# Kernel tuning notes

Measured on AMD Instinct MI355X. Metric: run time of the kernel, lower is better.

The kernel has to match this reference:

```python
import jax, jax.numpy as jnp
import numpy as np

B, N, E = 128, 50000, 1600000


def setup_inputs() -> dict:
    key = jax.random.key(0)
    k1, k2, k3, k4, k5 = jax.random.split(key, 5)
    x = jax.random.normal(k1, (B, N), dtype=jnp.float32)
    h = jax.random.normal(k2, (N,), dtype=jnp.float32)
    J = jax.random.normal(k3, (E,), dtype=jnp.float32)
    edge_idx_i = jax.random.randint(k4, (E,), 0, N, dtype=jnp.int64) if jax.config.jax_enable_x64 else jax.random.randint(k4, (E,), 0, N, dtype=jnp.int32)
    edge_idx_j = jax.random.randint(k5, (E,), 0, N, dtype=jnp.int32)
    return {"x": x, "h": h, "J": J, "edge_idx_i": edge_idx_i, "edge_idx_j": edge_idx_j}


def reference(x, h, J, edge_idx_i, edge_idx_j):
    # Hamiltonian: H(x) = x @ h + (x[:, ei] * x[:, ej]) @ J  -> shape (B,)
    interactions = x[:, edge_idx_i] * x[:, edge_idx_j]  # (B, E)
    return x @ h + interactions @ J
```

## Files before the change

### kernel.cpp

```cpp
#include <hip/hip_runtime.h>
#include <hip/hip_bf16.h>
#include <hip/hip_fp16.h>

#define BDIM    128
#define NGROUPS 2
#define GCOLS   64
#define ROWB    (GCOLS * 2)
#define EBLK    2048
#define RANKS   (EBLK / NGROUPS)
#define CHUNK   256
#define S1BLK   (NGROUPS * 8)
#define HBLK2   8
#define RPS     (RANKS / 8)
#define TPAD    132

__global__ __launch_bounds__(256) void transpose_h_kernel(
    const float* __restrict__ x, const float* __restrict__ h,
    __half* __restrict__ xTh, float* __restrict__ hp, int N) {
  __shared__ float tile[64 * TPAD];
  __shared__ float sh[64];
  __shared__ float red2[2][BDIM];
  const int tid = threadIdx.x;
  const int n0  = blockIdx.x * 64;

  const int c     = tid & 15;
  const int b0    = tid >> 4;
  const int nbase = n0 + 4 * c;
#pragma unroll
  for (int p = 0; p < 8; ++p) {
    const int b = b0 + 16 * p;
    float4 v;
    if (nbase + 3 < N) {
      v = *(const float4*)&x[(size_t)b * N + nbase];
    } else {
      v.x = (nbase + 0 < N) ? x[(size_t)b * N + nbase + 0] : 0.f;
      v.y = (nbase + 1 < N) ? x[(size_t)b * N + nbase + 1] : 0.f;
      v.z = (nbase + 2 < N) ? x[(size_t)b * N + nbase + 2] : 0.f;
      v.w = (nbase + 3 < N) ? x[(size_t)b * N + nbase + 3] : 0.f;
    }
    tile[(4 * c + 0) * TPAD + b] = v.x;
    tile[(4 * c + 1) * TPAD + b] = v.y;
    tile[(4 * c + 2) * TPAD + b] = v.z;
    tile[(4 * c + 3) * TPAD + b] = v.w;
  }
  if (tid < 64) sh[tid] = (n0 + tid < N) ? h[n0 + tid] : 0.f;
  __syncthreads();

  const int hb   = tid & 127;
  const int half = tid >> 7;
  float hacc = 0.f;
#pragma unroll
  for (int m = 0; m < 32; ++m) {
    const int nl = half * 32 + m;
    hacc += tile[nl * TPAD + hb] * sh[nl];
  }
  red2[half][hb] = hacc;

  const int oct = tid & 7;
  const int g2  = (tid >> 3) & 1;
  const int r0  = tid >> 4;
#pragma unroll
  for (int p = 0; p < 4; ++p) {
    const int nl = r0 + 16 * p;
    const int n  = n0 + nl;
    if (n < N) {
      const float* src = &tile[nl * TPAD + g2 * GCOLS + oct * 8];
      const float4 lo = *(const float4*)(src);
      const float4 hi = *(const float4*)(src + 4);
      int4 outv;
      outv.x = __builtin_bit_cast(int, __floats2half2_rn(lo.x, lo.y));
      outv.y = __builtin_bit_cast(int, __floats2half2_rn(lo.z, lo.w));
      outv.z = __builtin_bit_cast(int, __floats2half2_rn(hi.x, hi.y));
      outv.w = __builtin_bit_cast(int, __floats2half2_rn(hi.z, hi.w));
      *(int4*)(xTh + ((size_t)g2 * N + n) * GCOLS + oct * 8) = outv;
    }
  }
  __syncthreads();
  if (tid < BDIM) hp[(size_t)blockIdx.x * BDIM + tid] = red2[0][tid] + red2[1][tid];
}

__device__ __forceinline__ void fma8mix(float* acc, int4 vi, int4 vj, float Jv) {
  const int wi[4] = {vi.x, vi.y, vi.z, vi.w};
  const int wj[4] = {vj.x, vj.y, vj.z, vj.w};
#pragma unroll
  for (int w = 0; w < 4; ++w) {
    const __half2 hi = __builtin_bit_cast(__half2, wi[w]);
    const __half2 hj = __builtin_bit_cast(__half2, wj[w]);
    const int p = __builtin_bit_cast(int, __hmul2(hi, hj));
    asm("v_fma_mix_f32 %0, %1, %2, %0 op_sel_hi:[1,0,0]"
        : "+v"(acc[2 * w]) : "v"(p), "v"(Jv));
    asm("v_fma_mix_f32 %0, %1, %2, %0 op_sel:[1,0,0] op_sel_hi:[1,0,0]"
        : "+v"(acc[2 * w + 1]) : "v"(p), "v"(Jv));
  }
}

__global__ __launch_bounds__(256, 4) void edge_kernel(
    const __half* __restrict__ xTh, const float* __restrict__ J,
    const int* __restrict__ ei, const int* __restrict__ ej,
    float* __restrict__ P, int E, int N) {
  const int tid  = threadIdx.x;
  const int g    = (blockIdx.x & 7) >> 2;
  const int rank = (blockIdx.x >> 3) * 4 + (blockIdx.x & 3);
  const int wave = tid >> 6;
  const int lane = tid & 63;
  const int k    = lane >> 3;
  const char* xgl = (const char*)xTh + (size_t)g * N * ROWB + (lane & 7) * 16;

  const int TC    = (E + CHUNK - 1) / CHUNK;
  const int start = (int)(((long)rank * TC / RANKS)) * CHUNK;
  const int end   = min((int)(((long)(rank + 1) * TC / RANKS)) * CHUNK, E);

  __shared__ int4 se[CHUNK];

  int ri = 0, rj = 0;
  float rJ = 0.f;
  {
    const int e = start + tid;
    if (e < end) { ri = ei[e]; rj = ej[e]; rJ = J[e]; }
  }

  float acc[8] = {0.f, 0.f, 0.f, 0.f, 0.f, 0.f, 0.f, 0.f};

  for (int base = start; base < end; base += CHUNK) {
    se[tid] = make_int4(ri, rj, __float_as_int(rJ), 0);
    __syncthreads();

    {
      const int e = base + CHUNK + tid;
      ri = 0; rj = 0; rJ = 0.f;
      if (e < end) { ri = ei[e]; rj = ej[e]; rJ = J[e]; }
    }

    const int lbase = wave * 64 + k;
    const int4 eA0 = se[lbase + 0 * 8];
    const int4 eA1 = se[lbase + 1 * 8];
    const int4 eA2 = se[lbase + 2 * 8];
    const int4 eA3 = se[lbase + 3 * 8];
    const int4 viA0 = *(const int4*)(xgl + (unsigned)eA0.x * ROWB);
    const int4 vjA0 = *(const int4*)(xgl + (unsigned)eA0.y * ROWB);
    const int4 viA1 = *(const int4*)(xgl + (unsigned)eA1.x * ROWB);
    const int4 vjA1 = *(const int4*)(xgl + (unsigned)eA1.y * ROWB);
    const int4 viA2 = *(const int4*)(xgl + (unsigned)eA2.x * ROWB);
    const int4 vjA2 = *(const int4*)(xgl + (unsigned)eA2.y * ROWB);
    const int4 viA3 = *(const int4*)(xgl + (unsigned)eA3.x * ROWB);
    const int4 vjA3 = *(const int4*)(xgl + (unsigned)eA3.y * ROWB);
    const int4 eB0 = se[lbase + 4 * 8];
    const int4 eB1 = se[lbase + 5 * 8];
    const int4 eB2 = se[lbase + 6 * 8];
    const int4 eB3 = se[lbase + 7 * 8];
    const int4 viB0 = *(const int4*)(xgl + (unsigned)eB0.x * ROWB);
    const int4 vjB0 = *(const int4*)(xgl + (unsigned)eB0.y * ROWB);
    const int4 viB1 = *(const int4*)(xgl + (unsigned)eB1.x * ROWB);
    const int4 vjB1 = *(const int4*)(xgl + (unsigned)eB1.y * ROWB);
    const int4 viB2 = *(const int4*)(xgl + (unsigned)eB2.x * ROWB);
    const int4 vjB2 = *(const int4*)(xgl + (unsigned)eB2.y * ROWB);
    const int4 viB3 = *(const int4*)(xgl + (unsigned)eB3.x * ROWB);
    const int4 vjB3 = *(const int4*)(xgl + (unsigned)eB3.y * ROWB);
    __builtin_amdgcn_sched_barrier(0);
    fma8mix(acc, viA0, vjA0, __int_as_float(eA0.z));
    fma8mix(acc, viA1, vjA1, __int_as_float(eA1.z));
    fma8mix(acc, viA2, vjA2, __int_as_float(eA2.z));
    fma8mix(acc, viA3, vjA3, __int_as_float(eA3.z));
    fma8mix(acc, viB0, vjB0, __int_as_float(eB0.z));
    fma8mix(acc, viB1, vjB1, __int_as_float(eB1.z));
    fma8mix(acc, viB2, vjB2, __int_as_float(eB2.z));
    fma8mix(acc, viB3, vjB3, __int_as_float(eB3.z));
    __syncthreads();
  }

#pragma unroll
  for (int off = 8; off < 64; off <<= 1)
#pragma unroll
    for (int w = 0; w < 8; ++w) acc[w] += __shfl_xor(acc[w], off);

  __shared__ float red[4][GCOLS];
  if (lane < 8)
#pragma unroll
    for (int w = 0; w < 8; ++w) red[wave][lane * 8 + w] = acc[w];
  __syncthreads();
  if (tid < GCOLS) {
    const float s = red[0][tid] + red[1][tid] + red[2][tid] + red[3][tid];
    P[((size_t)g * RANKS + rank) * GCOLS + tid] = s;
  }
}

__global__ __launch_bounds__(256) void reduce1_kernel(
    const float* __restrict__ P, const float* __restrict__ hp,
    float* __restrict__ P2, float* __restrict__ hp2, int hrows) {
  __shared__ float red[4][GCOLS];
  __shared__ float redh[2][BDIM];
  if (blockIdx.x < S1BLK) {
    const int g  = blockIdx.x >> 3;
    const int s  = blockIdx.x & 7;
    const int rl = threadIdx.x >> 6;
    const int c  = threadIdx.x & 63;
    float acc = 0.f;
    for (int rr = rl; rr < RPS; rr += 4)
      acc += P[((size_t)g * RANKS + s * RPS + rr) * GCOLS + c];
    red[rl][c] = acc;
    __syncthreads();
    if (threadIdx.x < GCOLS) {
      float sum = 0.f;
      for (int r = 0; r < 4; ++r) sum += red[r][threadIdx.x];
      P2[(size_t)blockIdx.x * GCOLS + threadIdx.x] = sum;
    }
  } else {
    const int s  = blockIdx.x - S1BLK;
    const int b  = threadIdx.x & 127;
    const int rg = threadIdx.x >> 7;
    float acc = 0.f;
    for (int r = s + 8 * rg; r < hrows; r += 16)
      acc += hp[(size_t)r * BDIM + b];
    redh[rg][b] = acc;
    __syncthreads();
    if (threadIdx.x < BDIM)
      hp2[(size_t)s * BDIM + threadIdx.x] = redh[0][threadIdx.x] + redh[1][threadIdx.x];
  }
}

__global__ __launch_bounds__(128) void reduce2_kernel(
    const float* __restrict__ P2, const float* __restrict__ hp2,
    float* __restrict__ out) {
  const int b = threadIdx.x;
  const int g = b >> 6;
  const int c = b & 63;
  float acc = 0.f;
  for (int s = 0; s < 8; ++s) acc += hp2[(size_t)s * BDIM + b];
  for (int s = 0; s < 8; ++s) acc += P2[(size_t)(g * 8 + s) * GCOLS + c];
  out[b] = acc;
}

extern "C" void kernel_launch(void* const* d_in, const int* in_sizes, int n_in,
                              void* d_out, int out_size, void* d_ws, size_t ws_size,
                              hipStream_t stream) {
  const float* x  = (const float*)d_in[0];
  const float* h  = (const float*)d_in[1];
  const float* J  = (const float*)d_in[2];
  const int*   ei = (const int*)d_in[3];
  const int*   ej = (const int*)d_in[4];
  float* out = (float*)d_out;

  const int N = in_sizes[1];
  const int E = in_sizes[2];

  const int tblocks = (N + 63) / 64;

  __half* xTh = (__half*)d_ws;
  float* P   = (float*)(xTh + (size_t)NGROUPS * N * GCOLS);
  float* P2  = P   + (size_t)NGROUPS * RANKS * GCOLS;
  float* hp  = P2  + (size_t)S1BLK * GCOLS;
  float* hp2 = hp  + (size_t)tblocks * BDIM;

  transpose_h_kernel<<<tblocks, 256, 0, stream>>>(x, h, xTh, hp, N);

  edge_kernel<<<EBLK, 256, 0, stream>>>(xTh, J, ei, ej, P, E, N);

  reduce1_kernel<<<S1BLK + HBLK2, 256, 0, stream>>>(P, hp, P2, hp2, tblocks);

  reduce2_kernel<<<1, BDIM, 0, stream>>>(P2, hp2, out);
}
```

Baseline: 80.81 us.

## Partition edges per wave and broadcast indices via shuffles instead of LDS

Each wave now owns its own contiguous range of 64-edge chunks instead of the block sharing 256-edge chunks staged through shared memory. Edge indices and weights are prefetched into registers per lane and distributed with wave shuffles, which removes the LDS staging and both __syncthreads per iteration. This lets waves progress independently and avoids barrier stalls. The cost is 24 shuffles per iteration and finer-grained load balance that may leave some waves with one more chunk than others.

```diff
diff --git a/kernel.cpp b/kernel.cpp
--- a/kernel.cpp
+++ b/kernel.cpp
@@ -8,7 +8,7 @@
 #define ROWB    (GCOLS * 2)
 #define EBLK    2048
 #define RANKS   (EBLK / NGROUPS)
-#define CHUNK   256
+#define WPG     (RANKS * 4)
 #define S1BLK   (NGROUPS * 8)
 #define HBLK2   8
 #define RPS     (RANKS / 8)
@@ -106,66 +106,71 @@
   const int k    = lane >> 3;
   const char* xgl = (const char*)xTh + (size_t)g * N * ROWB + (lane & 7) * 16;
 
-  const int TC    = (E + CHUNK - 1) / CHUNK;
-  const int start = (int)(((long)rank * TC / RANKS)) * CHUNK;
-  const int end   = min((int)(((long)(rank + 1) * TC / RANKS)) * CHUNK, E);
-
-  __shared__ int4 se[CHUNK];
+  const int  wi   = rank * 4 + wave;
+  const long TC   = (E + 63) >> 6;
+  int base = (int)((long)wi * TC / WPG) * 64;
+  const int bend = (int)((long)(wi + 1) * TC / WPG) * 64;
+
+  float acc[8] = {0.f, 0.f, 0.f, 0.f, 0.f, 0.f, 0.f, 0.f};
 
   int ri = 0, rj = 0;
   float rJ = 0.f;
-  {
-    const int e = start + tid;
-    if (e < end) { ri = ei[e]; rj = ej[e]; rJ = J[e]; }
-  }
-
-  float acc[8] = {0.f, 0.f, 0.f, 0.f, 0.f, 0.f, 0.f, 0.f};
-
-  for (int base = start; base < end; base += CHUNK) {
-    se[tid] = make_int4(ri, rj, __float_as_int(rJ), 0);
-    __syncthreads();
-
+  if (base < bend) {
+    const int e  = base + lane;
+    const int ec = min(e, E - 1);
+    ri = ei[ec]; rj = ej[ec]; rJ = (e < E) ? J[ec] : 0.f;
+  }
+
+  for (; base < bend; base += 64) {
+    const int ci = ri, cj = rj;
+    const float cJ = rJ;
     {
-      const int e = base + CHUNK + tid;
-      ri = 0; rj = 0; rJ = 0.f;
-      if (e < end) { ri = ei[e]; rj = ej[e]; rJ = J[e]; }
-    }
-
-    const int lbase = wave * 64 + k;
-    const int4 eA0 = se[lbase + 0 * 8];
-    const int4 eA1 = se[lbase + 1 * 8];
-    const int4 eA2 = se[lbase + 2 * 8];
-    const int4 eA3 = se[lbase + 3 * 8];
-    const int4 viA0 = *(const int4*)(xgl + (unsigned)eA0.x * ROWB);
-    const int4 vjA0 = *(const int4*)(xgl + (unsigned)eA0.y * ROWB);
-    const int4 viA1 = *(const int4*)(xgl + (unsigned)eA1.x * ROWB);
-    const int4 vjA1 = *(const int4*)(xgl + (unsigned)eA1.y * ROWB);
-    const int4 viA2 = *(const int4*)(xgl + (unsigned)eA2.x * ROWB);
-    const int4 vjA2 = *(const int4*)(xgl + (unsigned)eA2.y * ROWB);
-    const int4 viA3 = *(const int4*)(xgl + (unsigned)eA3.x * ROWB);
-    const int4 vjA3 = *(const int4*)(xgl + (unsigned)eA3.y * ROWB);
-    const int4 eB0 = se[lbase + 4 * 8];
-    const int4 eB1 = se[lbase + 5 * 8];
-    const int4 eB2 = se[lbase + 6 * 8];
-    const int4 eB3 = se[lbase + 7 * 8];
-    const int4 viB0 = *(const int4*)(xgl + (unsigned)eB0.x * ROWB);
-    const int4 vjB0 = *(const int4*)(xgl + (unsigned)eB0.y * ROWB);
-    const int4 viB1 = *(const int4*)(xgl + (unsigned)eB1.x * ROWB);
-    const int4 vjB1 = *(const int4*)(xgl + (unsigned)eB1.y * ROWB);
-    const int4 viB2 = *(const int4*)(xgl + (unsigned)eB2.x * ROWB);
-    const int4 vjB2 = *(const int4*)(xgl + (unsigned)eB2.y * ROWB);
-    const int4 viB3 = *(const int4*)(xgl + (unsigned)eB3.x * ROWB);
-    const int4 vjB3 = *(const int4*)(xgl + (unsigned)eB3.y * ROWB);
+      const int nb = base + 64;
+      if (nb < bend) {
+        const int e  = nb + lane;
+        const int ec = min(e, E - 1);
+        ri = ei[ec]; rj = ej[ec]; rJ = (e < E) ? J[ec] : 0.f;
+      }
+    }
+
+    const int   i0 = __shfl(ci, 0 * 8 + k), j0 = __shfl(cj, 0 * 8 + k);
+    const int   i1 = __shfl(ci, 1 * 8 + k), j1 = __shfl(cj, 1 * 8 + k);
+    const int   i2 = __shfl(ci, 2 * 8 + k), j2 = __shfl(cj, 2 * 8 + k);
+    const int   i3 = __shfl(ci, 3 * 8 + k), j3 = __shfl(cj, 3 * 8 + k);
+    const int   i4 = __shfl(ci, 4 * 8 + k), j4 = __shfl(cj, 4 * 8 + k);
+    const int   i5 = __shfl(ci, 5 * 8 + k), j5 = __shfl(cj, 5 * 8 + k);
+    const int   i6 = __shfl(ci, 6 * 8 + k), j6 = __shfl(cj, 6 * 8 + k);
+    const int   i7 = __shfl(ci, 7 * 8 + k), j7 = __shfl(cj, 7 * 8 + k);
+    const float J0 = __shfl(cJ, 0 * 8 + k), J1 = __shfl(cJ, 1 * 8 + k);
+    const float J2 = __shfl(cJ, 2 * 8 + k), J3 = __shfl(cJ, 3 * 8 + k);
+    const float J4 = __shfl(cJ, 4 * 8 + k), J5 = __shfl(cJ, 5 * 8 + k);
+    const float J6 = __shfl(cJ, 6 * 8 + k), J7 = __shfl(cJ, 7 * 8 + k);
+
+    const int4 vi0 = *(const int4*)(xgl + (unsigned)i0 * ROWB);
+    const int4 vj0 = *(const int4*)(xgl + (unsigned)j0 * ROWB);
+    const int4 vi1 = *(const int4*)(xgl + (unsigned)i1 * ROWB);
+    const int4 vj1 = *(const int4*)(xgl + (unsigned)j1 * ROWB);
+    const int4 vi2 = *(const int4*)(xgl + (unsigned)i2 * ROWB);
+    const int4 vj2 = *(const int4*)(xgl + (unsigned)j2 * ROWB);
+    const int4 vi3 = *(const int4*)(xgl + (unsigned)i3 * ROWB);
+    const int4 vj3 = *(const int4*)(xgl + (unsigned)j3 * ROWB);
+    const int4 vi4 = *(const int4*)(xgl + (unsigned)i4 * ROWB);
+    const int4 vj4 = *(const int4*)(xgl + (unsigned)j4 * ROWB);
+    const int4 vi5 = *(const int4*)(xgl + (unsigned)i5 * ROWB);
+    const int4 vj5 = *(const int4*)(xgl + (unsigned)j5 * ROWB);
+    const int4 vi6 = *(const int4*)(xgl + (unsigned)i6 * ROWB);
+    const int4 vj6 = *(const int4*)(xgl + (unsigned)j6 * ROWB);
+    const int4 vi7 = *(const int4*)(xgl + (unsigned)i7 * ROWB);
+    const int4 vj7 = *(const int4*)(xgl + (unsigned)j7 * ROWB);
     __builtin_amdgcn_sched_barrier(0);
-    fma8mix(acc, viA0, vjA0, __int_as_float(eA0.z));
-    fma8mix(acc, viA1, vjA1, __int_as_float(eA1.z));
-    fma8mix(acc, viA2, vjA2, __int_as_float(eA2.z));
-    fma8mix(acc, viA3, vjA3, __int_as_float(eA3.z));
-    fma8mix(acc, viB0, vjB0, __int_as_float(eB0.z));
-    fma8mix(acc, viB1, vjB1, __int_as_float(eB1.z));
-    fma8mix(acc, viB2, vjB2, __int_as_float(eB2.z));
-    fma8mix(acc, viB3, vjB3, __int_as_float(eB3.z));
-    __syncthreads();
+    fma8mix(acc, vi0, vj0, J0);
+    fma8mix(acc, vi1, vj1, J1);
+    fma8mix(acc, vi2, vj2, J2);
+    fma8mix(acc, vi3, vj3, J3);
+    fma8mix(acc, vi4, vj4, J4);
+    fma8mix(acc, vi5, vj5, J5);
+    fma8mix(acc, vi6, vj6, J6);
+    fma8mix(acc, vi7, vj7, J7);
   }
 
 #pragma unroll
```

After: 79.53 us. Within noise of the previous version (-1.6%).
